# Kernel tuning notes

Hardware: AMD Instinct MI355X
Metric: run time of the kernel (lower is better)

## Reference

```python
import jax, jax.numpy as jnp
import numpy as np

B, N, E, H = 8, 2000, 20, 128


def setup_inputs() -> dict:
    key = jax.random.key(0)
    ks = jax.random.split(key, 9)
    s = 1.0 / np.sqrt(H)
    return {
        "x": jax.random.normal(ks[0], (B, N, H), dtype=jnp.float32),
        "e": jax.random.normal(ks[1], (B, N * E, H), dtype=jnp.float32),
        "Wu": jax.random.uniform(ks[2], (H, H), jnp.float32, -s, s),
        "bu": jax.random.uniform(ks[3], (H,), jnp.float32, -s, s),
        "Wv": jax.random.uniform(ks[4], (H, H), jnp.float32, -s, s),
        "bv": jax.random.uniform(ks[5], (H,), jnp.float32, -s, s),
        "We": jax.random.uniform(ks[6], (H, H), jnp.float32, -s, s),
        "be": jax.random.uniform(ks[7], (H,), jnp.float32, -s, s),
        "edge_index": jax.random.randint(ks[8], (B, N * E), 0, N, dtype=jnp.int32),
        "n_edges": E,
    }


def reference(x, e, Wu, bu, Wv, bv, We, be, edge_index, n_edges):
    b, n, h = x.shape
    Ux = x @ Wu + bu                      # [B, N, H] node self-embedding
    Vx = x @ Wv + bv                      # [B, N, H] neighbor embedding
    Ve = e @ We + be                      # [B, N*E, H] edge embedding
    # softmax over the n_edges axis per (node, channel)
    Ve = jax.nn.softmax(Ve.reshape(b, n, n_edges, h), axis=2)
    # gather neighbor features along node axis via edge_index
    Vx_g = jnp.take_along_axis(Vx, edge_index[..., None], axis=1)  # [B, N*E, H]
    to = (Ve * Vx_g.reshape(b, n, n_edges, h)).sum(axis=2)          # [B, N, H]
    return Ux + to
```

## Files before the change

kernel.cpp:

```cpp
#include <hip/hip_runtime.h>

#define B_   8
#define NN   2000
#define EE   20
#define HH   128
#define BN   (B_*NN)
#define NE   (NN*EE)

typedef unsigned short ushort_t;
typedef __bf16 bf16x8 __attribute__((ext_vector_type(8)));
typedef float  f32x4  __attribute__((ext_vector_type(4)));
typedef float  f4     __attribute__((ext_vector_type(4)));
typedef unsigned short us8 __attribute__((ext_vector_type(8)));
typedef unsigned short us4 __attribute__((ext_vector_type(4)));

union FragU { us8 u; bf16x8 b; };

__device__ __forceinline__ float b2f(ushort_t v) {
    union { unsigned int i; float f; } c; c.i = ((unsigned int)v) << 16; return c.f;
}
__device__ __forceinline__ ushort_t f2b(float f) {
    union { float f; unsigned int i; } c; c.f = f;
    unsigned int r = (c.i + 0x7FFFu + ((c.i >> 16) & 1u)) >> 16;
    return (ushort_t)r;
}

__global__ __launch_bounds__(256) void k0_prep(
    const float* __restrict__ Wu, const float* __restrict__ Wv,
    const float* __restrict__ We,
    ushort_t* __restrict__ WuT, ushort_t* __restrict__ WvT,
    ushort_t* __restrict__ WeT)
{
    __shared__ ushort_t lds[128 * 130];
    const int bid = blockIdx.x;
    const float* W = (bid == 0) ? Wu : (bid == 1) ? Wv : We;
    ushort_t*   WT = (bid == 0) ? WuT : (bid == 1) ? WvT : WeT;
#pragma unroll
    for (int it = 0; it < 64; ++it) {
        int c = it * 256 + threadIdx.x;
        lds[(c >> 7) * 130 + (c & 127)] = f2b(W[c]);
    }
    __syncthreads();
#pragma unroll
    for (int it = 0; it < 64; ++it) {
        int o = it * 256 + threadIdx.x;
        WT[o] = lds[(o & 127) * 130 + (o >> 7)];
    }
}

__global__ __launch_bounds__(256, 4) void k1_embed(
    const float* __restrict__ x,
    const ushort_t* __restrict__ WuT, const float* __restrict__ bu,
    const ushort_t* __restrict__ WvT, const float* __restrict__ bv,
    ushort_t* __restrict__ Uxb, ushort_t* __restrict__ Vxb)
{
    const int tid  = threadIdx.x;
    const int lane = tid & 63;
    const int wave = tid >> 6;
    const int wm = wave >> 1, wn = wave & 1;
    const int q  = lane >> 4, ln = lane & 15;
    const int m0 = blockIdx.x * 64;
    const int sel = blockIdx.y;
    const ushort_t* WT   = sel ? WvT : WuT;
    const float*    bias = sel ? bv : bu;
    ushort_t* dst = sel ? Vxb : Uxb;

    FragU bf[4][4];
#pragma unroll
    for (int ki = 0; ki < 4; ++ki)
#pragma unroll
        for (int tn = 0; tn < 4; ++tn)
            bf[ki][tn].u = *(const us8*)(WT + (size_t)(wn * 64 + tn * 16 + ln) * HH + ki * 32 + q * 8);

    f32x4 acc[2][4];
#pragma unroll
    for (int tm = 0; tm < 2; ++tm)
#pragma unroll
        for (int tn = 0; tn < 4; ++tn) acc[tm][tn] = (f32x4){0.f, 0.f, 0.f, 0.f};

#pragma unroll
    for (int ki = 0; ki < 4; ++ki) {
        FragU af[2];
#pragma unroll
        for (int tm = 0; tm < 2; ++tm) {
            const float* p = x + (size_t)(m0 + wm * 32 + tm * 16 + ln) * HH + ki * 32 + q * 8;
            f4 lo = *(const f4*)(p);
            f4 hi = *(const f4*)(p + 4);
            us8 t;
#pragma unroll
            for (int r = 0; r < 4; ++r) { t[r] = f2b(lo[r]); t[r + 4] = f2b(hi[r]); }
            af[tm].u = t;
        }
#pragma unroll
        for (int tm = 0; tm < 2; ++tm)
#pragma unroll
            for (int tn = 0; tn < 4; ++tn)
                acc[tm][tn] = __builtin_amdgcn_mfma_f32_16x16x32_bf16(
                    af[tm].b, bf[ki][tn].b, acc[tm][tn], 0, 0, 0);
    }

#pragma unroll
    for (int tn = 0; tn < 4; ++tn) {
        int col = wn * 64 + tn * 16 + ln;
        float bb = bias[col];
#pragma unroll
        for (int tm = 0; tm < 2; ++tm) {
            int rowb = m0 + wm * 32 + tm * 16 + q * 4;
#pragma unroll
            for (int r = 0; r < 4; ++r)
                dst[(size_t)(rowb + r) * HH + col] = f2b(acc[tm][tn][r] + bb);
        }
    }
}

#define CSTR 84

__global__ __launch_bounds__(256, 4) void k2_fused(
    const float* __restrict__ e, const ushort_t* __restrict__ WeT,
    const int* __restrict__ eidx,
    const ushort_t* __restrict__ Uxb, const ushort_t* __restrict__ Vxb,
    float* __restrict__ out)
{
    __shared__ __align__(16) ushort_t ct[128 * CSTR];

    const int tid  = threadIdx.x;
    const int lane = tid & 63;
    const int wave = tid >> 6;
    const int q  = lane >> 4, ln = lane & 15;

    const int b   = blockIdx.y;
    const int nl0 = blockIdx.x * 4;
    const size_t erow0 = (size_t)b * NE + (size_t)nl0 * EE;
    const float* ebase = e + erow0 * HH;

    FragU bf[4][2];
#pragma unroll
    for (int ki = 0; ki < 4; ++ki)
#pragma unroll
        for (int tn = 0; tn < 2; ++tn)
            bf[ki][tn].u = *(const us8*)(WeT + (size_t)(wave * 32 + tn * 16 + ln) * HH + ki * 32 + q * 8);

    f32x4 acc[5][2];
#pragma unroll
    for (int tm = 0; tm < 5; ++tm)
#pragma unroll
        for (int tn = 0; tn < 2; ++tn) acc[tm][tn] = (f32x4){0.f, 0.f, 0.f, 0.f};

#pragma unroll
    for (int ki = 0; ki < 4; ++ki) {
        FragU af[5];
#pragma unroll
        for (int tm = 0; tm < 5; ++tm) {
            const float* p = ebase + (size_t)(tm * 16 + ln) * HH + ki * 32 + q * 8;
            f4 lo = *(const f4*)(p);
            f4 hi = *(const f4*)(p + 4);
            us8 t;
#pragma unroll
            for (int r = 0; r < 4; ++r) { t[r] = f2b(lo[r]); t[r + 4] = f2b(hi[r]); }
            af[tm].u = t;
        }
#pragma unroll
        for (int tm = 0; tm < 5; ++tm)
#pragma unroll
            for (int tn = 0; tn < 2; ++tn)
                acc[tm][tn] = __builtin_amdgcn_mfma_f32_16x16x32_bf16(
                    af[tm].b, bf[ki][tn].b, acc[tm][tn], 0, 0, 0);
    }

#pragma unroll
    for (int tm = 0; tm < 5; ++tm)
#pragma unroll
        for (int tn = 0; tn < 2; ++tn) {
            int col  = wave * 32 + tn * 16 + ln;
            int rowb = tm * 16 + q * 4;
            us4 pk;
#pragma unroll
            for (int r = 0; r < 4; ++r) pk[r] = f2b(acc[tm][tn][r]);
            *(us4*)(&ct[col * CSTR + rowb]) = pk;
        }

    const int hh = lane & 31;
    const int gh = lane >> 5;
    const int h  = wave * 32 + hh;
    const ushort_t* vbase = Vxb + (size_t)b * NN * HH + h;
    const int* ebidx = eidx + erow0;
#pragma unroll
    for (int j = 0; j < 2; ++j) {
        int g = gh + 2 * j;
        const ushort_t* ctp = &ct[h * CSTR + g * 20];
        float lv[20];
#pragma unroll
        for (int i = 0; i < 5; ++i) {
            us4 v = *(const us4*)(ctp + i * 4);
#pragma unroll
            for (int r = 0; r < 4; ++r) lv[i * 4 + r] = b2f(v[r]);
        }
        float mx = lv[0];
#pragma unroll
        for (int k = 1; k < EE; ++k) mx = fmaxf(mx, lv[k]);

        int idx[20];
#pragma unroll
        for (int k = 0; k < EE; ++k) idx[k] = ebidx[g * 20 + k];
        ushort_t gv[20];
#pragma unroll
        for (int k = 0; k < EE; ++k) gv[k] = vbase[(size_t)idx[k] * HH];

        float s = 0.f, a = 0.f;
#pragma unroll
        for (int k = 0; k < EE; ++k) {
            float p = __expf(lv[k] - mx);
            s += p;
            a = fmaf(p, b2f(gv[k]), a);
        }
        size_t orow = (size_t)(b * NN + nl0 + g) * HH + h;
        out[orow] = b2f(Uxb[orow]) + a / s;
    }
}

extern "C" void kernel_launch(void* const* d_in, const int* in_sizes, int n_in,
                              void* d_out, int out_size, void* d_ws, size_t ws_size,
                              hipStream_t stream) {
    const float* x  = (const float*)d_in[0];
    const float* e  = (const float*)d_in[1];
    const float* Wu = (const float*)d_in[2];
    const float* bu = (const float*)d_in[3];
    const float* Wv = (const float*)d_in[4];
    const float* bv = (const float*)d_in[5];
    const float* We = (const float*)d_in[6];
    const int*   eidx = (const int*)d_in[8];

    const size_t SZ = (size_t)BN * HH * 2;
    ushort_t* Uxb = (ushort_t*)d_ws;
    ushort_t* Vxb = (ushort_t*)((char*)d_ws + SZ);
    ushort_t* WuT = (ushort_t*)((char*)d_ws + 2 * SZ);
    ushort_t* WvT = WuT + HH * HH;
    ushort_t* WeT = WvT + HH * HH;
    float*    o   = (float*)d_out;

    k0_prep<<<dim3(3), 256, 0, stream>>>(Wu, Wv, We, WuT, WvT, WeT);
    k1_embed<<<dim3(250, 2), 256, 0, stream>>>(x, WuT, bu, WvT, bv, Uxb, Vxb);
    k2_fused<<<dim3(500, 8), 256, 0, stream>>>(e, WeT, eidx, Uxb, Vxb, o);
}
```

Measured before the change: 308.9 us.

## Stage edge tile in LDS, widen k2 to 512 threads, shrink k1 tiles

The fused edge kernel now loads the 80x128 edge tile cooperatively into LDS as bf16 once. Eight waves each compute a 16-column slice with MFMA from that LDS copy, where before each wave converted its own global reads. The gather/softmax phase maps one (node, channel) per thread and splits the 20 gathers into two batches of 10 to cut register pressure. k1 uses 16-row tiles with more blocks and higher occupancy bounds. The cost is extra LDS traffic and barriers in exchange for fewer redundant global loads and more parallelism.

```diff
diff --git a/kernel.cpp b/kernel.cpp
--- a/kernel.cpp
+++ b/kernel.cpp
@@ -48,7 +48,7 @@
     }
 }
 
-__global__ __launch_bounds__(256, 4) void k1_embed(
+__global__ __launch_bounds__(256, 8) void k1_embed(
     const float* __restrict__ x,
     const ushort_t* __restrict__ WuT, const float* __restrict__ bu,
     const ushort_t* __restrict__ WvT, const float* __restrict__ bv,
@@ -56,76 +56,59 @@
 {
     const int tid  = threadIdx.x;
     const int lane = tid & 63;
-    const int wave = tid >> 6;
-    const int wm = wave >> 1, wn = wave & 1;
+    const int w    = tid >> 6;
     const int q  = lane >> 4, ln = lane & 15;
-    const int m0 = blockIdx.x * 64;
+    const int m0 = blockIdx.x * 16;
     const int sel = blockIdx.y;
     const ushort_t* WT   = sel ? WvT : WuT;
     const float*    bias = sel ? bv : bu;
     ushort_t* dst = sel ? Vxb : Uxb;
 
-    FragU bf[4][4];
-#pragma unroll
-    for (int ki = 0; ki < 4; ++ki)
-#pragma unroll
-        for (int tn = 0; tn < 4; ++tn)
-            bf[ki][tn].u = *(const us8*)(WT + (size_t)(wn * 64 + tn * 16 + ln) * HH + ki * 32 + q * 8);
-
-    f32x4 acc[2][4];
-#pragma unroll
-    for (int tm = 0; tm < 2; ++tm)
-#pragma unroll
-        for (int tn = 0; tn < 4; ++tn) acc[tm][tn] = (f32x4){0.f, 0.f, 0.f, 0.f};
+    f32x4 acc[2];
+    acc[0] = (f32x4){0.f, 0.f, 0.f, 0.f};
+    acc[1] = (f32x4){0.f, 0.f, 0.f, 0.f};
 
 #pragma unroll
     for (int ki = 0; ki < 4; ++ki) {
-        FragU af[2];
-#pragma unroll
-        for (int tm = 0; tm < 2; ++tm) {
-            const float* p = x + (size_t)(m0 + wm * 32 + tm * 16 + ln) * HH + ki * 32 + q * 8;
-            f4 lo = *(const f4*)(p);
-            f4 hi = *(const f4*)(p + 4);
-            us8 t;
-#pragma unroll
-            for (int r = 0; r < 4; ++r) { t[r] = f2b(lo[r]); t[r + 4] = f2b(hi[r]); }
-            af[tm].u = t;
-        }
-#pragma unroll
-        for (int tm = 0; tm < 2; ++tm)
-#pragma unroll
-            for (int tn = 0; tn < 4; ++tn)
-                acc[tm][tn] = __builtin_amdgcn_mfma_f32_16x16x32_bf16(
-                    af[tm].b, bf[ki][tn].b, acc[tm][tn], 0, 0, 0);
-    }
-
-#pragma unroll
-    for (int tn = 0; tn < 4; ++tn) {
-        int col = wn * 64 + tn * 16 + ln;
+        const float* p = x + (size_t)(m0 + ln) * HH + ki * 32 + q * 8;
+        f4 lo = *(const f4*)(p);
+        f4 hi = *(const f4*)(p + 4);
+        FragU af;
+        us8 t;
+#pragma unroll
+        for (int r = 0; r < 4; ++r) { t[r] = f2b(lo[r]); t[r + 4] = f2b(hi[r]); }
+        af.u = t;
+        FragU bf0, bf1;
+        bf0.u = *(const us8*)(WT + (size_t)(w * 32 + ln) * HH + ki * 32 + q * 8);
+        bf1.u = *(const us8*)(WT + (size_t)(w * 32 + 16 + ln) * HH + ki * 32 + q * 8);
+        acc[0] = __builtin_amdgcn_mfma_f32_16x16x32_bf16(af.b, bf0.b, acc[0], 0, 0, 0);
+        acc[1] = __builtin_amdgcn_mfma_f32_16x16x32_bf16(af.b, bf1.b, acc[1], 0, 0, 0);
+    }
+
+#pragma unroll
+    for (int tn = 0; tn < 2; ++tn) {
+        int col = w * 32 + tn * 16 + ln;
         float bb = bias[col];
 #pragma unroll
-        for (int tm = 0; tm < 2; ++tm) {
-            int rowb = m0 + wm * 32 + tm * 16 + q * 4;
-#pragma unroll
-            for (int r = 0; r < 4; ++r)
-                dst[(size_t)(rowb + r) * HH + col] = f2b(acc[tm][tn][r] + bb);
-        }
-    }
-}
-
+        for (int r = 0; r < 4; ++r)
+            dst[(size_t)(m0 + q * 4 + r) * HH + col] = f2b(acc[tn][r] + bb);
+    }
+}
+
+#define ASTR 136
 #define CSTR 84
 
-__global__ __launch_bounds__(256, 4) void k2_fused(
+__global__ __launch_bounds__(512, 8) void k2_fused(
     const float* __restrict__ e, const ushort_t* __restrict__ WeT,
     const int* __restrict__ eidx,
     const ushort_t* __restrict__ Uxb, const ushort_t* __restrict__ Vxb,
     float* __restrict__ out)
 {
-    __shared__ __align__(16) ushort_t ct[128 * CSTR];
+    __shared__ __align__(16) ushort_t smem[80 * ASTR];
 
     const int tid  = threadIdx.x;
     const int lane = tid & 63;
-    const int wave = tid >> 6;
+    const int w    = tid >> 6;
     const int q  = lane >> 4, ln = lane & 15;
 
     const int b   = blockIdx.y;
@@ -133,89 +116,86 @@
     const size_t erow0 = (size_t)b * NE + (size_t)nl0 * EE;
     const float* ebase = e + erow0 * HH;
 
-    FragU bf[4][2];
-#pragma unroll
-    for (int ki = 0; ki < 4; ++ki)
-#pragma unroll
-        for (int tn = 0; tn < 2; ++tn)
-            bf[ki][tn].u = *(const us8*)(WeT + (size_t)(wave * 32 + tn * 16 + ln) * HH + ki * 32 + q * 8);
-
-    f32x4 acc[5][2];
-#pragma unroll
-    for (int tm = 0; tm < 5; ++tm)
-#pragma unroll
-        for (int tn = 0; tn < 2; ++tn) acc[tm][tn] = (f32x4){0.f, 0.f, 0.f, 0.f};
+#pragma unroll
+    for (int it = 0; it < 5; ++it) {
+        int c = it * 512 + tid;
+        int row = c >> 5, col = (c & 31) * 4;
+        f4 v = *(const f4*)(ebase + (size_t)row * HH + col);
+        us4 pk;
+#pragma unroll
+        for (int r = 0; r < 4; ++r) pk[r] = f2b(v[r]);
+        *(us4*)(&smem[row * ASTR + col]) = pk;
+    }
+
+    f32x4 acc[5];
+#pragma unroll
+    for (int tm = 0; tm < 5; ++tm) acc[tm] = (f32x4){0.f, 0.f, 0.f, 0.f};
+
+    __syncthreads();
 
 #pragma unroll
     for (int ki = 0; ki < 4; ++ki) {
+        FragU bf;
+        bf.u = *(const us8*)(WeT + (size_t)(w * 16 + ln) * HH + ki * 32 + q * 8);
         FragU af[5];
 #pragma unroll
+        for (int tm = 0; tm < 5; ++tm)
+            af[tm].u = *(const us8*)(&smem[(tm * 16 + ln) * ASTR + ki * 32 + q * 8]);
+#pragma unroll
+        for (int tm = 0; tm < 5; ++tm)
+            acc[tm] = __builtin_amdgcn_mfma_f32_16x16x32_bf16(af[tm].b, bf.b, acc[tm], 0, 0, 0);
+    }
+
+    __syncthreads();
+
+    {
+        int col = w * 16 + ln;
+#pragma unroll
         for (int tm = 0; tm < 5; ++tm) {
-            const float* p = ebase + (size_t)(tm * 16 + ln) * HH + ki * 32 + q * 8;
-            f4 lo = *(const f4*)(p);
-            f4 hi = *(const f4*)(p + 4);
-            us8 t;
-#pragma unroll
-            for (int r = 0; r < 4; ++r) { t[r] = f2b(lo[r]); t[r + 4] = f2b(hi[r]); }
-            af[tm].u = t;
+            us4 pk;
+#pragma unroll
+            for (int r = 0; r < 4; ++r) pk[r] = f2b(acc[tm][r]);
+            *(us4*)(&smem[col * CSTR + tm * 16 + q * 4]) = pk;
         }
-#pragma unroll
-        for (int tm = 0; tm < 5; ++tm)
-#pragma unroll
-            for (int tn = 0; tn < 2; ++tn)
-                acc[tm][tn] = __builtin_amdgcn_mfma_f32_16x16x32_bf16(
-                    af[tm].b, bf[ki][tn].b, acc[tm][tn], 0, 0, 0);
-    }
-
-#pragma unroll
-    for (int tm = 0; tm < 5; ++tm)
-#pragma unroll
-        for (int tn = 0; tn < 2; ++tn) {
-            int col  = wave * 32 + tn * 16 + ln;
-            int rowb = tm * 16 + q * 4;
-            us4 pk;
-#pragma unroll
-            for (int r = 0; r < 4; ++r) pk[r] = f2b(acc[tm][tn][r]);
-            *(us4*)(&ct[col * CSTR + rowb]) = pk;
-        }
-
-    const int hh = lane & 31;
-    const int gh = lane >> 5;
-    const int h  = wave * 32 + hh;
+    }
+
+    const int g = lane >> 4;
+    const int h = w * 16 + ln;
+    const int* ebidx = eidx + erow0 + g * EE;
     const ushort_t* vbase = Vxb + (size_t)b * NN * HH + h;
-    const int* ebidx = eidx + erow0;
-#pragma unroll
-    for (int j = 0; j < 2; ++j) {
-        int g = gh + 2 * j;
-        const ushort_t* ctp = &ct[h * CSTR + g * 20];
-        float lv[20];
+
+    float lv[20];
+    {
+        const ushort_t* ctp = &smem[h * CSTR + g * EE];
 #pragma unroll
         for (int i = 0; i < 5; ++i) {
             us4 v = *(const us4*)(ctp + i * 4);
 #pragma unroll
             for (int r = 0; r < 4; ++r) lv[i * 4 + r] = b2f(v[r]);
         }
-        float mx = lv[0];
-#pragma unroll
-        for (int k = 1; k < EE; ++k) mx = fmaxf(mx, lv[k]);
-
-        int idx[20];
-#pragma unroll
-        for (int k = 0; k < EE; ++k) idx[k] = ebidx[g * 20 + k];
-        ushort_t gv[20];
-#pragma unroll
-        for (int k = 0; k < EE; ++k) gv[k] = vbase[(size_t)idx[k] * HH];
-
-        float s = 0.f, a = 0.f;
-#pragma unroll
-        for (int k = 0; k < EE; ++k) {
-            float p = __expf(lv[k] - mx);
+    }
+    float mx = lv[0];
+#pragma unroll
+    for (int k = 1; k < EE; ++k) mx = fmaxf(mx, lv[k]);
+
+    float s = 0.f, a = 0.f;
+#pragma unroll
+    for (int half = 0; half < 2; ++half) {
+        int idx[10];
+#pragma unroll
+        for (int k = 0; k < 10; ++k) idx[k] = ebidx[half * 10 + k];
+        ushort_t gv[10];
+#pragma unroll
+        for (int k = 0; k < 10; ++k) gv[k] = vbase[(size_t)idx[k] * HH];
+#pragma unroll
+        for (int k = 0; k < 10; ++k) {
+            float p = __expf(lv[half * 10 + k] - mx);
             s += p;
             a = fmaf(p, b2f(gv[k]), a);
         }
-        size_t orow = (size_t)(b * NN + nl0 + g) * HH + h;
-        out[orow] = b2f(Uxb[orow]) + a / s;
-    }
+    }
+    size_t orow = (size_t)(b * NN + nl0 + g) * HH + h;
+    out[orow] = b2f(Uxb[orow]) + a / s;
 }
 
 extern "C" void kernel_launch(void* const* d_in, const int* in_sizes, int n_in,
@@ -239,6 +219,6 @@
     float*    o   = (float*)d_out;
 
     k0_prep<<<dim3(3), 256, 0, stream>>>(Wu, Wv, We, WuT, WvT, WeT);
-    k1_embed<<<dim3(250, 2), 256, 0, stream>>>(x, WuT, bu, WvT, bv, Uxb, Vxb);
-    k2_fused<<<dim3(500, 8), 256, 0, stream>>>(e, WeT, eidx, Uxb, Vxb, o);
-}
+    k1_embed<<<dim3(1000, 2), 256, 0, stream>>>(x, WuT, bu, WvT, bv, Uxb, Vxb);
+    k2_fused<<<dim3(500, 8), 512, 0, stream>>>(e, WeT, eidx, Uxb, Vxb, o);
+}
```

Measured after the change: 276.9 us. -10.4%, faster.
